# Kernel tuning notes

Measured on AMD Instinct MI355X. Metric: run time of the kernel, lower is better.

Reference implementation:

```python
import jax, jax.numpy as jnp
import numpy as np

KS = 3          # deformable kernel size
PAD = 1         # zero padding
N = KS * KS     # sample points per pixel


def conv2d(x, w, b=None, padding=1):
    out = jax.lax.conv_general_dilated(
        x, w, (1, 1), [(padding, padding)] * 2,
        dimension_numbers=('NCHW', 'OIHW', 'NCHW'))
    if b is not None:
        out = out + b[None, :, None, None]
    return out


def setup_inputs() -> dict:
    key = jax.random.key(0)
    k0, k1, k2, k3 = jax.random.split(key, 4)
    B, C, H, W, O = 4, 64, 128, 128, 64
    x = jax.random.normal(k0, (B, C, H, W), jnp.float32)
    # p_conv / m_conv are zero-init in the original; use small random weights
    # so offsets/modulation are non-trivial but sampling stays local.
    w_p = jax.random.normal(k1, (2 * N, C, 3, 3), jnp.float32) * 0.01
    b_p = jnp.zeros((2 * N,), jnp.float32)
    w_m = jax.random.normal(k2, (N, C, 3, 3), jnp.float32) * 0.01
    b_m = jnp.zeros((N,), jnp.float32)
    w_conv = jax.random.normal(k3, (O, C, KS, KS), jnp.float32) / np.sqrt(C * N)
    return {'x': x, 'w_p': w_p, 'b_p': b_p, 'w_m': w_m, 'b_m': b_m, 'w_conv': w_conv}


def reference(x, w_p, b_p, w_m, b_m, w_conv):
    B, C, H, W = x.shape
    offset = conv2d(x, w_p, b_p)              # (B, 2N, H, W): first N rows(x), last N cols(y)
    m = jax.nn.sigmoid(conv2d(x, w_m, b_m))   # (B, N, H, W) modulation
    xp = jnp.pad(x, ((0, 0), (0, 0), (PAD, PAD), (PAD, PAD)))  # zero_padding
    Hp, Wp = H + 2 * PAD, W + 2 * PAD

    # p = p_0 + p_n + offset  (coords in padded image, p_0 starts at 1)
    r = (KS - 1) // 2
    pn_x, pn_y = jnp.meshgrid(jnp.arange(-r, r + 1), jnp.arange(-r, r + 1), indexing='ij')
    pn = jnp.concatenate([pn_x.reshape(-1), pn_y.reshape(-1)]).astype(x.dtype)          # (2N,)
    p0_x, p0_y = jnp.meshgrid(jnp.arange(1, H + 1), jnp.arange(1, W + 1), indexing='ij')
    p0 = jnp.concatenate([jnp.tile(p0_x[None], (N, 1, 1)),
                          jnp.tile(p0_y[None], (N, 1, 1))], 0).astype(x.dtype)           # (2N,H,W)
    p = offset + pn[None, :, None, None] + p0[None]
    p = jnp.moveaxis(p, 1, -1)                # (B,H,W,2N)

    fx = jnp.floor(jax.lax.stop_gradient(p[..., :N]))  # p.detach().floor()
    fy = jnp.floor(jax.lax.stop_gradient(p[..., N:]))
    q_lt_x = jnp.clip(fx, 0, Hp - 1).astype(jnp.int32)
    q_lt_y = jnp.clip(fy, 0, Wp - 1).astype(jnp.int32)
    q_rb_x = jnp.clip(fx + 1, 0, Hp - 1).astype(jnp.int32)
    q_rb_y = jnp.clip(fy + 1, 0, Wp - 1).astype(jnp.int32)
    px = jnp.clip(p[..., :N], 0, Hp - 1)
    py = jnp.clip(p[..., N:], 0, Wp - 1)

    # bilinear kernel weights (same algebra as torch version)
    g_lt = (1 + (q_lt_x - px)) * (1 + (q_lt_y - py))
    g_rb = (1 - (q_rb_x - px)) * (1 - (q_rb_y - py))
    g_lb = (1 + (q_lt_x - px)) * (1 - (q_rb_y - py))
    g_rt = (1 - (q_rb_x - px)) * (1 + (q_lt_y - py))

    xf = xp.reshape(B, C, Hp * Wp)

    def gather(qx, qy):
        idx = (qx * Wp + qy).reshape(B, 1, -1)                      # (B,1,H*W*N)
        return jnp.take_along_axis(xf, idx, axis=2).reshape(B, C, H, W, N)

    x_off = (g_lt[:, None] * gather(q_lt_x, q_lt_y)
             + g_rb[:, None] * gather(q_rb_x, q_rb_y)
             + g_lb[:, None] * gather(q_lt_x, q_rb_y)
             + g_rt[:, None] * gather(q_rb_x, q_lt_y))               # (B,C,H,W,N)

    x_off = x_off * jnp.moveaxis(m, 1, -1)[:, None]                  # modulation (DCNv2)

    # _reshape_x_offset + conv(kernel=ks, stride=ks) == einsum over the N samples
    out = jnp.einsum('bchwk,ock->bohw', x_off,
                     w_conv.reshape(w_conv.shape[0], C, N))
    return out
```

## Files before the change

### kernel.cpp

```cpp
#include <hip/hip_runtime.h>
#include <hip/hip_bf16.h>

#define BB 4
#define CC 64
#define HH 128
#define WW 128
#define OO 64
#define NN 9
#define HW 16384
#define HP 130
#define WP 130

#define WPMB_F  0
#define BPM_OFF 9216
#define WCB_F   9248
#define XT_F    27680
#define PX_OFF  2124832
#define PSZ     589824

typedef __attribute__((ext_vector_type(8))) short s8v;
typedef __attribute__((ext_vector_type(8))) unsigned short u8v;
typedef __attribute__((ext_vector_type(4))) float f4v;

__device__ __forceinline__ unsigned short f2bu(float f) {
    unsigned int b = __float_as_uint(f);
    return (unsigned short)((b + 0x7FFFu + ((b >> 16) & 1u)) >> 16);
}
__device__ __forceinline__ float bu2f(unsigned short u) {
    return __uint_as_float(((unsigned int)u) << 16);
}

__global__ void k_prep(const float* __restrict__ wp,
                       const float* __restrict__ bp,
                       const float* __restrict__ wm,
                       const float* __restrict__ bm,
                       const float* __restrict__ wcv,
                       float* __restrict__ ws) {
    int tid = blockIdx.x * blockDim.x + threadIdx.x;
    if (tid < 18432) {
        int r = tid / 576;
        int kk = tid % 576;
        int kt = kk >> 6;
        int c = kk & 63;
        int dy = kt / 3, dx = kt % 3;
        float v = 0.f;
        if (r < 18)       v = wp[((r * 64 + c) * 3 + dy) * 3 + dx];
        else if (r < 27)  v = wm[(((r - 18) * 64 + c) * 3 + dy) * 3 + dx];
        ((unsigned short*)(ws + WPMB_F))[tid] = f2bu(v);
    } else if (tid < 18459) {
        int i = tid - 18432;
        ws[BPM_OFF + i] = (i < 18) ? bp[i] : bm[i - 18];
    } else if (tid >= 20480 && tid < 20480 + 36864) {
        int d = tid - 20480;
        int o = d / 576;
        int kk = d % 576;
        int kt = kk >> 6;
        int c = kk & 63;
        ((unsigned short*)(ws + WCB_F))[o * 576 + kk] = f2bu(wcv[(o * 64 + c) * 9 + kt]);
    }
}

__global__ void __launch_bounds__(256) k_xt(const float* __restrict__ x,
                                            float* __restrict__ ws) {
    __shared__ unsigned short tile[64][66];
    int blk = blockIdx.x;
    int b = blk >> 8;
    int hw0 = (blk & 255) * 64;
    int t = threadIdx.x;
    unsigned short* xt = (unsigned short*)(ws + XT_F);

#pragma unroll
    for (int p = 0; p < 16; p++) {
        int c = p * 4 + (t >> 6);
        int i = t & 63;
        tile[c][i] = f2bu(x[((size_t)(b * 64 + c)) * HW + hw0 + i]);
    }
    __syncthreads();
#pragma unroll
    for (int p = 0; p < 16; p++) {
        int i = p * 4 + (t >> 6);
        int c = t & 63;
        xt[((size_t)(b * HW + hw0 + i)) * 64 + c] = tile[c][i];
    }
}

__global__ void __launch_bounds__(256) k_off(const float* __restrict__ ws,
                                             float* __restrict__ wsout) {
    __shared__ unsigned short Awld[32 * 72];
    __shared__ unsigned short Bld[64 * 72];

    int t = threadIdx.x;
    int lane = t & 63;
    int wid = t >> 6;
    int ln15 = lane & 15;
    int quad = lane >> 4;

    int blk = blockIdx.x;
    int b = blk >> 8;
    int hw0 = (blk & 255) * 64;

    const unsigned short* wpmb = (const unsigned short*)(ws + WPMB_F);
    const unsigned short* xtb = (const unsigned short*)(ws + XT_F) + (size_t)b * HW * 64;
    const float* bpm = ws + BPM_OFF;

    int aq_row = t >> 3, aq_g = t & 7;
    int bq_pix = t & 63, bq_half = t >> 6;
    int ph = (hw0 + bq_pix) >> 7;
    int pw = (hw0 + bq_pix) & 127;

    f4v acc[2];
    acc[0] = (f4v){0.f, 0.f, 0.f, 0.f};
    acc[1] = (f4v){0.f, 0.f, 0.f, 0.f};

#pragma unroll 1
    for (int kt = 0; kt < 9; kt++) {
        int dy = kt / 3, dx = kt % 3;
        __syncthreads();
        {
            u8v av = *(const u8v*)(wpmb + aq_row * 576 + kt * 64 + aq_g * 8);
            *(u8v*)(&Awld[aq_row * 72 + aq_g * 8]) = av;
        }
        {
            int h2 = ph + dy - 1, w2 = pw + dx - 1;
            bool val = ((unsigned)h2 < 128u) && ((unsigned)w2 < 128u);
            u8v z = (u8v){0, 0, 0, 0, 0, 0, 0, 0};
            u8v e0 = z, e1 = z;
            if (val) {
                const unsigned short* src = xtb + ((size_t)(h2 * 128 + w2)) * 64 + bq_half * 16;
                e0 = *(const u8v*)(src);
                e1 = *(const u8v*)(src + 8);
            }
            *(u8v*)(&Bld[bq_pix * 72 + bq_half * 16]) = e0;
            *(u8v*)(&Bld[bq_pix * 72 + bq_half * 16 + 8]) = e1;
        }
        __syncthreads();

#pragma unroll
        for (int ks = 0; ks < 2; ks++) {
            s8v bf = *(const s8v*)(&Bld[(wid * 16 + ln15) * 72 + ks * 32 + quad * 8]);
#pragma unroll
            for (int mt = 0; mt < 2; mt++) {
                s8v af = *(const s8v*)(&Awld[(mt * 16 + ln15) * 72 + ks * 32 + quad * 8]);
                acc[mt] = __builtin_amdgcn_mfma_f32_16x16x32_bf16(af, bf, acc[mt], 0, 0, 0);
            }
        }
    }

    int p = hw0 + wid * 16 + ln15;
    int h = p >> 7, w = p & 127;
    float* pxA = wsout + PX_OFF;
    float* pyA = pxA + PSZ;
    float* mmA = pyA + PSZ;
#pragma unroll
    for (int mt = 0; mt < 2; mt++) {
#pragma unroll
        for (int r = 0; r < 4; r++) {
            int oc = mt * 16 + quad * 4 + r;
            if (oc < 27) {
                float v = acc[mt][r] + bpm[oc];
                if (oc < 9) {
                    int ki = oc / 3;
                    pxA[((size_t)b * NN + oc) * HW + p] = v + (float)(ki - 1) + (float)(h + 1);
                } else if (oc < 18) {
                    int k = oc - 9;
                    int kj = k % 3;
                    pyA[((size_t)b * NN + k) * HW + p] = v + (float)(kj - 1) + (float)(w + 1);
                } else {
                    int k = oc - 18;
                    mmA[((size_t)b * NN + k) * HW + p] = 1.f / (1.f + __expf(-v));
                }
            }
        }
    }
}

__global__ void __launch_bounds__(256) k_gemm(const float* __restrict__ ws,
                                              float* __restrict__ out) {
    __shared__ unsigned short Ald[64 * 72];
    __shared__ unsigned short Sld[64 * 72];

    int t = threadIdx.x;
    int lane = t & 63;
    int wid = t >> 6;
    int ln15 = lane & 15;
    int quad = lane >> 4;

    int blk = blockIdx.x;
    int b = blk >> 8;
    int hw0 = (blk & 255) * 64;

    const unsigned short* wcb = (const unsigned short*)(ws + WCB_F);
    const unsigned short* xtb = (const unsigned short*)(ws + XT_F) + (size_t)b * HW * 64;
    const float* pxA = ws + PX_OFF;
    const float* pyA = pxA + PSZ;
    const float* mmA = pyA + PSZ;

    int p_loc = t >> 2;
    int cq = t & 3;

    f4v acc[4];
#pragma unroll
    for (int mt = 0; mt < 4; mt++) acc[mt] = (f4v){0.f, 0.f, 0.f, 0.f};

#pragma unroll 1
    for (int kt = 0; kt < 9; kt++) {
        size_t pidx = ((size_t)b * NN + kt) * HW + hw0 + p_loc;
        float px = pxA[pidx];
        float py = pyA[pidx];
        float mk = mmA[pidx];

        float fx = floorf(px), fy = floorf(py);
        float pxc = fminf(fmaxf(px, 0.f), (float)(HP - 1));
        float pyc = fminf(fmaxf(py, 0.f), (float)(WP - 1));
        int qltx = (int)fminf(fmaxf(fx, 0.f), (float)(HP - 1));
        int qlty = (int)fminf(fmaxf(fy, 0.f), (float)(WP - 1));
        int qrbx = (int)fminf(fmaxf(fx + 1.f, 0.f), (float)(HP - 1));
        int qrby = (int)fminf(fmaxf(fy + 1.f, 0.f), (float)(WP - 1));

        float gltx = 1.f + ((float)qltx - pxc);
        float glty = 1.f + ((float)qlty - pyc);
        float grbx = 1.f - ((float)qrbx - pxc);
        float grby = 1.f - ((float)qrby - pyc);

        bool vlx = (qltx >= 1) && (qltx <= HH);
        bool vly = (qlty >= 1) && (qlty <= WW);
        bool vrx = (qrbx >= 1) && (qrbx <= HH);
        bool vry = (qrby >= 1) && (qrby <= WW);
        float g0 = (vlx && vly) ? gltx * glty * mk : 0.f;
        float g1 = (vrx && vry) ? grbx * grby * mk : 0.f;
        float g2 = (vlx && vry) ? gltx * grby * mk : 0.f;
        float g3 = (vrx && vly) ? grbx * glty * mk : 0.f;

        int xlt = min(max(qltx - 1, 0), HH - 1);
        int ylt = min(max(qlty - 1, 0), WW - 1);
        int xrb = min(max(qrbx - 1, 0), HH - 1);
        int yrb = min(max(qrby - 1, 0), WW - 1);
        size_t i0 = (size_t)(xlt * WW + ylt) * 64;
        size_t i1 = (size_t)(xrb * WW + yrb) * 64;
        size_t i2 = (size_t)(xlt * WW + yrb) * 64;
        size_t i3 = (size_t)(xrb * WW + ylt) * 64;

        __syncthreads();
        {
            int row = t >> 2, g = t & 3;
            const unsigned short* src = wcb + row * 576 + kt * 64 + g * 16;
            *(u8v*)(&Ald[row * 72 + g * 16]) = *(const u8v*)(src);
            *(u8v*)(&Ald[row * 72 + g * 16 + 8]) = *(const u8v*)(src + 8);
        }
        {
            int cbase = cq * 16;
            const unsigned short* s0 = xtb + i0 + cbase;
            const unsigned short* s1 = xtb + i1 + cbase;
            const unsigned short* s2 = xtb + i2 + cbase;
            const unsigned short* s3 = xtb + i3 + cbase;
            u8v e0a = *(const u8v*)(s0), e0b = *(const u8v*)(s0 + 8);
            u8v e1a = *(const u8v*)(s1), e1b = *(const u8v*)(s1 + 8);
            u8v e2a = *(const u8v*)(s2), e2b = *(const u8v*)(s2 + 8);
            u8v e3a = *(const u8v*)(s3), e3b = *(const u8v*)(s3 + 8);
            u8v sva, svb;
#pragma unroll
            for (int j = 0; j < 8; j++) {
                float va = g0 * bu2f(e0a[j]) + g1 * bu2f(e1a[j])
                         + g2 * bu2f(e2a[j]) + g3 * bu2f(e3a[j]);
                float vb = g0 * bu2f(e0b[j]) + g1 * bu2f(e1b[j])
                         + g2 * bu2f(e2b[j]) + g3 * bu2f(e3b[j]);
                sva[j] = f2bu(va);
                svb[j] = f2bu(vb);
            }
            *(u8v*)(&Sld[p_loc * 72 + cbase]) = sva;
            *(u8v*)(&Sld[p_loc * 72 + cbase + 8]) = svb;
        }
        __syncthreads();

#pragma unroll
        for (int ks = 0; ks < 2; ks++) {
            s8v bf = *(const s8v*)(&Sld[(wid * 16 + ln15) * 72 + ks * 32 + quad * 8]);
#pragma unroll
            for (int mt = 0; mt < 4; mt++) {
                s8v af = *(const s8v*)(&Ald[(mt * 16 + ln15) * 72 + ks * 32 + quad * 8]);
                acc[mt] = __builtin_amdgcn_mfma_f32_16x16x32_bf16(af, bf, acc[mt], 0, 0, 0);
            }
        }
    }

    int pix = hw0 + wid * 16 + ln15;
    float* ob = out + (size_t)b * (OO * HW) + pix;
#pragma unroll
    for (int mt = 0; mt < 4; mt++) {
#pragma unroll
        for (int r = 0; r < 4; r++) {
            ob[(size_t)(mt * 16 + quad * 4 + r) * HW] = acc[mt][r];
        }
    }
}

extern "C" void kernel_launch(void* const* d_in, const int* in_sizes, int n_in,
                              void* d_out, int out_size, void* d_ws, size_t ws_size,
                              hipStream_t stream) {
    const float* x   = (const float*)d_in[0];
    const float* wp  = (const float*)d_in[1];
    const float* bp  = (const float*)d_in[2];
    const float* wm  = (const float*)d_in[3];
    const float* bm  = (const float*)d_in[4];
    const float* wcv = (const float*)d_in[5];
    float* ws = (float*)d_ws;
    float* out = (float*)d_out;

    hipLaunchKernelGGL(k_prep, dim3(224), dim3(256), 0, stream, wp, bp, wm, bm, wcv, ws);
    hipLaunchKernelGGL(k_xt, dim3(1024), dim3(256), 0, stream, x, ws);
    hipLaunchKernelGGL(k_off, dim3(1024), dim3(256), 0, stream, ws, ws);
    hipLaunchKernelGGL(k_gemm, dim3(1024), dim3(256), 0, stream, ws, out);
}
```

Before: 121.3 us.

## Fuse offset conv and deformable gather-GEMM into one kernel with LDS halo

Merges the offset/modulation convolution kernel into the sampling GEMM kernel. Offsets and masks stay in LDS instead of being written to and re-read from global workspace. The offset conv now loads a 3x66 pixel halo tile once and reuses it across all nine taps, rather than reloading shifted inputs each tap. Its weights are read directly from global memory instead of being staged in LDS. In exchange, LDS use per block rises to about 35KB, which may lower occupancy.

```diff
diff --git a/kernel.cpp b/kernel.cpp
--- a/kernel.cpp
+++ b/kernel.cpp
@@ -15,8 +15,6 @@
 #define BPM_OFF 9216
 #define WCB_F   9248
 #define XT_F    27680
-#define PX_OFF  2124832
-#define PSZ     589824
 
 typedef __attribute__((ext_vector_type(8))) short s8v;
 typedef __attribute__((ext_vector_type(8))) unsigned short u8v;
@@ -84,10 +82,13 @@
     }
 }
 
-__global__ void __launch_bounds__(256) k_off(const float* __restrict__ ws,
-                                             float* __restrict__ wsout) {
-    __shared__ unsigned short Awld[32 * 72];
-    __shared__ unsigned short Bld[64 * 72];
+__global__ void __launch_bounds__(256) k_fused(const float* __restrict__ ws,
+                                               float* __restrict__ out) {
+    __shared__ char ldsbuf[35424];
+    unsigned short* halo = (unsigned short*)ldsbuf;
+    unsigned short* Sld  = (unsigned short*)ldsbuf;
+    unsigned short* A2ld = (unsigned short*)(ldsbuf + 9216);
+    float* pm = (float*)(ldsbuf + 28512);
 
     int t = threadIdx.x;
     int lane = t & 63;
@@ -98,102 +99,84 @@
     int blk = blockIdx.x;
     int b = blk >> 8;
     int hw0 = (blk & 255) * 64;
+    int h = hw0 >> 7;
+    int w0 = hw0 & 127;
 
     const unsigned short* wpmb = (const unsigned short*)(ws + WPMB_F);
-    const unsigned short* xtb = (const unsigned short*)(ws + XT_F) + (size_t)b * HW * 64;
+    const unsigned short* wcb  = (const unsigned short*)(ws + WCB_F);
+    const unsigned short* xtb  = (const unsigned short*)(ws + XT_F) + (size_t)b * HW * 64;
     const float* bpm = ws + BPM_OFF;
 
-    int aq_row = t >> 3, aq_g = t & 7;
-    int bq_pix = t & 63, bq_half = t >> 6;
-    int ph = (hw0 + bq_pix) >> 7;
-    int pw = (hw0 + bq_pix) & 127;
-
-    f4v acc[2];
-    acc[0] = (f4v){0.f, 0.f, 0.f, 0.f};
-    acc[1] = (f4v){0.f, 0.f, 0.f, 0.f};
+    {
+        u8v z = (u8v){0, 0, 0, 0, 0, 0, 0, 0};
+#pragma unroll
+        for (int i = 0; i < 4; i++) {
+            int s = t + i * 256;
+            if (s < 792) {
+                int cg = s & 3;
+                int rc = s >> 2;
+                int col = rc % 66;
+                int r = rc / 66;
+                int h2 = h + r - 1;
+                int w2 = w0 + col - 1;
+                bool val = ((unsigned)h2 < 128u) && ((unsigned)w2 < 128u);
+                u8v e0 = z, e1 = z;
+                if (val) {
+                    const unsigned short* src = xtb + ((size_t)(h2 * 128 + w2)) * 64 + cg * 16;
+                    e0 = *(const u8v*)(src);
+                    e1 = *(const u8v*)(src + 8);
+                }
+                unsigned short* dst = halo + (r * 66 + col) * 72 + cg * 16;
+                *(u8v*)(dst) = e0;
+                *(u8v*)(dst + 8) = e1;
+            }
+        }
+    }
+    __syncthreads();
+
+    f4v acc1[2];
+    acc1[0] = (f4v){0.f, 0.f, 0.f, 0.f};
+    acc1[1] = (f4v){0.f, 0.f, 0.f, 0.f};
 
 #pragma unroll 1
     for (int kt = 0; kt < 9; kt++) {
         int dy = kt / 3, dx = kt % 3;
-        __syncthreads();
-        {
-            u8v av = *(const u8v*)(wpmb + aq_row * 576 + kt * 64 + aq_g * 8);
-            *(u8v*)(&Awld[aq_row * 72 + aq_g * 8]) = av;
-        }
-        {
-            int h2 = ph + dy - 1, w2 = pw + dx - 1;
-            bool val = ((unsigned)h2 < 128u) && ((unsigned)w2 < 128u);
-            u8v z = (u8v){0, 0, 0, 0, 0, 0, 0, 0};
-            u8v e0 = z, e1 = z;
-            if (val) {
-                const unsigned short* src = xtb + ((size_t)(h2 * 128 + w2)) * 64 + bq_half * 16;
-                e0 = *(const u8v*)(src);
-                e1 = *(const u8v*)(src + 8);
-            }
-            *(u8v*)(&Bld[bq_pix * 72 + bq_half * 16]) = e0;
-            *(u8v*)(&Bld[bq_pix * 72 + bq_half * 16 + 8]) = e1;
-        }
-        __syncthreads();
-
 #pragma unroll
         for (int ks = 0; ks < 2; ks++) {
-            s8v bf = *(const s8v*)(&Bld[(wid * 16 + ln15) * 72 + ks * 32 + quad * 8]);
+            int cs = ks * 32 + quad * 8;
+            s8v bf = *(const s8v*)(&halo[(dy * 66 + wid * 16 + ln15 + dx) * 72 + cs]);
 #pragma unroll
             for (int mt = 0; mt < 2; mt++) {
-                s8v af = *(const s8v*)(&Awld[(mt * 16 + ln15) * 72 + ks * 32 + quad * 8]);
-                acc[mt] = __builtin_amdgcn_mfma_f32_16x16x32_bf16(af, bf, acc[mt], 0, 0, 0);
-            }
-        }
-    }
-
-    int p = hw0 + wid * 16 + ln15;
-    int h = p >> 7, w = p & 127;
-    float* pxA = wsout + PX_OFF;
-    float* pyA = pxA + PSZ;
-    float* mmA = pyA + PSZ;
-#pragma unroll
-    for (int mt = 0; mt < 2; mt++) {
-#pragma unroll
-        for (int r = 0; r < 4; r++) {
-            int oc = mt * 16 + quad * 4 + r;
-            if (oc < 27) {
-                float v = acc[mt][r] + bpm[oc];
-                if (oc < 9) {
-                    int ki = oc / 3;
-                    pxA[((size_t)b * NN + oc) * HW + p] = v + (float)(ki - 1) + (float)(h + 1);
-                } else if (oc < 18) {
-                    int k = oc - 9;
-                    int kj = k % 3;
-                    pyA[((size_t)b * NN + k) * HW + p] = v + (float)(kj - 1) + (float)(w + 1);
-                } else {
-                    int k = oc - 18;
-                    mmA[((size_t)b * NN + k) * HW + p] = 1.f / (1.f + __expf(-v));
+                s8v af = *(const s8v*)(wpmb + (mt * 16 + ln15) * 576 + kt * 64 + cs);
+                acc1[mt] = __builtin_amdgcn_mfma_f32_16x16x32_bf16(af, bf, acc1[mt], 0, 0, 0);
+            }
+        }
+    }
+
+    {
+        int n = wid * 16 + ln15;
+        int pw = w0 + n;
+#pragma unroll
+        for (int mt = 0; mt < 2; mt++) {
+#pragma unroll
+            for (int r = 0; r < 4; r++) {
+                int oc = mt * 16 + quad * 4 + r;
+                if (oc < 27) {
+                    float v = acc1[mt][r] + bpm[oc];
+                    if (oc < 9) {
+                        v += (float)(oc / 3 - 1) + (float)(h + 1);
+                    } else if (oc < 18) {
+                        int k = oc - 9;
+                        v += (float)(k % 3 - 1) + (float)(pw + 1);
+                    } else {
+                        v = 1.f / (1.f + __expf(-v));
+                    }
+                    pm[oc * 64 + n] = v;
                 }
             }
         }
     }
-}
-
-__global__ void __launch_bounds__(256) k_gemm(const float* __restrict__ ws,
-                                              float* __restrict__ out) {
-    __shared__ unsigned short Ald[64 * 72];
-    __shared__ unsigned short Sld[64 * 72];
-
-    int t = threadIdx.x;
-    int lane = t & 63;
-    int wid = t >> 6;
-    int ln15 = lane & 15;
-    int quad = lane >> 4;
-
-    int blk = blockIdx.x;
-    int b = blk >> 8;
-    int hw0 = (blk & 255) * 64;
-
-    const unsigned short* wcb = (const unsigned short*)(ws + WCB_F);
-    const unsigned short* xtb = (const unsigned short*)(ws + XT_F) + (size_t)b * HW * 64;
-    const float* pxA = ws + PX_OFF;
-    const float* pyA = pxA + PSZ;
-    const float* mmA = pyA + PSZ;
+    __syncthreads();
 
     int p_loc = t >> 2;
     int cq = t & 3;
@@ -204,10 +187,9 @@
 
 #pragma unroll 1
     for (int kt = 0; kt < 9; kt++) {
-        size_t pidx = ((size_t)b * NN + kt) * HW + hw0 + p_loc;
-        float px = pxA[pidx];
-        float py = pyA[pidx];
-        float mk = mmA[pidx];
+        float px = pm[kt * 64 + p_loc];
+        float py = pm[(9 + kt) * 64 + p_loc];
+        float mk = pm[(18 + kt) * 64 + p_loc];
 
         float fx = floorf(px), fy = floorf(py);
         float pxc = fminf(fmaxf(px, 0.f), (float)(HP - 1));
@@ -244,8 +226,8 @@
         {
             int row = t >> 2, g = t & 3;
             const unsigned short* src = wcb + row * 576 + kt * 64 + g * 16;
-            *(u8v*)(&Ald[row * 72 + g * 16]) = *(const u8v*)(src);
-            *(u8v*)(&Ald[row * 72 + g * 16 + 8]) = *(const u8v*)(src + 8);
+            *(u8v*)(&A2ld[row * 72 + g * 16]) = *(const u8v*)(src);
+            *(u8v*)(&A2ld[row * 72 + g * 16 + 8]) = *(const u8v*)(src + 8);
         }
         {
             int cbase = cq * 16;
@@ -277,7 +259,7 @@
             s8v bf = *(const s8v*)(&Sld[(wid * 16 + ln15) * 72 + ks * 32 + quad * 8]);
 #pragma unroll
             for (int mt = 0; mt < 4; mt++) {
-                s8v af = *(const s8v*)(&Ald[(mt * 16 + ln15) * 72 + ks * 32 + quad * 8]);
+                s8v af = *(const s8v*)(&A2ld[(mt * 16 + ln15) * 72 + ks * 32 + quad * 8]);
                 acc[mt] = __builtin_amdgcn_mfma_f32_16x16x32_bf16(af, bf, acc[mt], 0, 0, 0);
             }
         }
@@ -308,6 +290,5 @@
 
     hipLaunchKernelGGL(k_prep, dim3(224), dim3(256), 0, stream, wp, bp, wm, bm, wcv, ws);
     hipLaunchKernelGGL(k_xt, dim3(1024), dim3(256), 0, stream, x, ws);
-    hipLaunchKernelGGL(k_off, dim3(1024), dim3(256), 0, stream, ws, ws);
-    hipLaunchKernelGGL(k_gemm, dim3(1024), dim3(256), 0, stream, ws, out);
-}
+    hipLaunchKernelGGL(k_fused, dim3(1024), dim3(256), 0, stream, ws, out);
+}
```

Result: slower. 124.5 us (+2.7%).
